# Kernel optimization log

Hardware: AMD Instinct MI355X
Metric: run time of the kernel (lower is better)

Reference implementation:

```python
import jax, jax.numpy as jnp
import numpy as np

B, T, NM = 32, 128, 53
IN_DIM, H, L = 3, 256, 64
K = 1024
HEADS, DH = 8, 64
INNER = HEADS * DH  # 512 (dim_head*heads, independent of H as in source)
COMMIT = 0.25


def _conv1d(x, w, b):
    # x: [B, C, T], w: [O, I, 3] (torch Conv1d layout), padding=1 == SAME for k=3
    y = jax.lax.conv_general_dilated(x, w, (1,), 'SAME',
                                     dimension_numbers=('NCH', 'OIH', 'NCH'))
    return y + b[None, :, None]


def setup_inputs():
    key = jax.random.key(0)
    ks = jax.random.split(key, 20)
    g = lambda i, shape: jax.random.normal(ks[i], shape, jnp.float32) * 0.02
    return dict(
        x=jax.random.normal(ks[0], (B, T, NM, IN_DIM), jnp.float32),
        seeds=jax.random.normal(ks[1], (B * T, NM, H), jnp.float32) * 0.02,
        enc_mlp_w1=g(2, (IN_DIM, H)), enc_mlp_b1=jnp.zeros((H,), jnp.float32),
        enc_mlp_w2=g(3, (H, H)), enc_mlp_b2=jnp.zeros((H,), jnp.float32),
        enc_qkv_w=g(4, (H, 3 * INNER)),
        enc_out_w=g(5, (INNER, H)), enc_out_b=jnp.zeros((H,), jnp.float32),
        enc_conv1_w=g(6, (H, H, 3)), enc_conv1_b=jnp.zeros((H,), jnp.float32),
        enc_conv2_w=g(7, (H, H, 3)), enc_conv2_b=jnp.zeros((H,), jnp.float32),
        enc_proj_w=g(8, (H, L)), enc_proj_b=jnp.zeros((L,), jnp.float32),
        codebook=jax.random.uniform(ks[9], (K, L), jnp.float32, -1.0 / K, 1.0 / K),
        dec_init_w=g(10, (L, H)), dec_init_b=jnp.zeros((H,), jnp.float32),
        dec_conv1_w=g(11, (H, H, 3)), dec_conv1_b=jnp.zeros((H,), jnp.float32),
        dec_conv2_w=g(12, (H, H, 3)), dec_conv2_b=jnp.zeros((H,), jnp.float32),
        dec_gen_w1=g(13, (H, H)), dec_gen_b1=jnp.zeros((H,), jnp.float32),
        dec_gen_w2=g(14, (H, H)), dec_gen_b2=jnp.zeros((H,), jnp.float32),
        dec_gen_w3=g(15, (H, IN_DIM)), dec_gen_b3=jnp.zeros((IN_DIM,), jnp.float32),
    )


def reference(x, seeds, enc_mlp_w1, enc_mlp_b1, enc_mlp_w2, enc_mlp_b2,
              enc_qkv_w, enc_out_w, enc_out_b,
              enc_conv1_w, enc_conv1_b, enc_conv2_w, enc_conv2_b,
              enc_proj_w, enc_proj_b, codebook,
              dec_init_w, dec_init_b,
              dec_conv1_w, dec_conv1_b, dec_conv2_w, dec_conv2_b,
              dec_gen_w1, dec_gen_b1, dec_gen_w2, dec_gen_b2,
              dec_gen_w3, dec_gen_b3):
    b, t, nm, _ = x.shape
    # ---- encoder ----
    h = x.reshape(b * t, nm, -1)
    h = jax.nn.relu(h @ enc_mlp_w1 + enc_mlp_b1)
    h = jax.nn.relu(h @ enc_mlp_w2 + enc_mlp_b2)
    qkv = h @ enc_qkv_w  # [(bt), nm, 3*INNER], no bias
    q, k_, v = jnp.split(qkv, 3, axis=-1)
    split_heads = lambda a: a.reshape(b * t, nm, HEADS, DH).transpose(0, 2, 1, 3)
    q, k_, v = split_heads(q), split_heads(k_), split_heads(v)
    dots = jnp.einsum('mhid,mhjd->mhij', q, k_) * (DH ** -0.5)
    attn = jax.nn.softmax(dots, axis=-1)
    o = jnp.einsum('mhij,mhjd->mhid', attn, v)
    o = o.transpose(0, 2, 1, 3).reshape(b * t, nm, INNER)
    h = o @ enc_out_w + enc_out_b
    h = h.mean(axis=1)                               # [(bt), H]
    h = h.reshape(b, t, -1).transpose(0, 2, 1)       # [b, H, t]
    h = jax.nn.relu(_conv1d(h, enc_conv1_w, enc_conv1_b))
    h = jax.nn.relu(_conv1d(h, enc_conv2_w, enc_conv2_b))
    z = h.transpose(0, 2, 1) @ enc_proj_w + enc_proj_b  # [b, t, L]
    # ---- vector quantizer (faithful to source: distance expression is only
    # the ||x||^2 term -> [M,1]; argmin over size-1 axis -> index 0 always) ----
    flat = z.reshape(-1, L)
    distances = jnp.sum(flat ** 2, axis=1, keepdims=True)  # [M, 1]
    idx = jnp.argmin(distances, axis=1)                    # all zeros
    encodings = jax.nn.one_hot(idx, K, dtype=z.dtype)      # [M, K]
    quantized = (encodings @ codebook).reshape(z.shape)
    e_loss = jnp.mean((jax.lax.stop_gradient(quantized) - z) ** 2)
    q_loss = jnp.mean((quantized - jax.lax.stop_gradient(z)) ** 2)
    vq_loss = q_loss + COMMIT * e_loss
    z_q = z + jax.lax.stop_gradient(quantized - z)  # straight-through
    avg_probs = jnp.mean(encodings, axis=0)
    perplexity = jnp.exp(-jnp.sum(avg_probs * jnp.log(avg_probs + 1e-10)))
    # ---- decoder ----
    d = z_q @ dec_init_w + dec_init_b                # [b, t, H]
    d = d.transpose(0, 2, 1)
    d = jax.nn.relu(_conv1d(d, dec_conv1_w, dec_conv1_b))
    d = jax.nn.relu(_conv1d(d, dec_conv2_w, dec_conv2_b))
    d = d.transpose(0, 2, 1).reshape(b * t, -1)      # [(bt), H]
    p = d[:, None, :] + seeds                        # [(bt), NM, H]
    p = jax.nn.relu(p @ dec_gen_w1 + dec_gen_b1)
    p = jax.nn.relu(p @ dec_gen_w2 + dec_gen_b2)
    p = p @ dec_gen_w3 + dec_gen_b3
    recon = p.reshape(b, t, NM, -1)
    return recon, vq_loss, perplexity
```

## Files before the change

### kernel.cpp

```cpp
#include <hip/hip_runtime.h>
#include <cstdint>
#include <cstddef>

#define NM    53
#define NMP   56
#define HD    256
#define BTT   4096

typedef __attribute__((ext_vector_type(8))) short short8v;
typedef __attribute__((ext_vector_type(4))) float f32x4;
#define MFMA16(a,b,c) __builtin_amdgcn_mfma_f32_16x16x32_bf16(a,b,c,0,0,0)

__device__ __forceinline__ float4 ldg4(const float* p) { return *(const float4*)p; }

__device__ __forceinline__ short f2bf(float f){
    union { float f; uint32_t u; } v; v.f = f;
    uint32_t r = v.u + 0x7fff + ((v.u >> 16) & 1);
    return (short)(r >> 16);
}
__device__ __forceinline__ float bf2f(short s){
    union { uint32_t u; float f; } v; v.u = ((uint32_t)(uint16_t)s) << 16;
    return v.f;
}

__global__ void k_prep_bf16(const float* __restrict__ w2, const float* __restrict__ wqkv,
                            const float* __restrict__ g1, const float* __restrict__ g2,
                            const float* __restrict__ g3,
                            short* __restrict__ w2T, short* __restrict__ wqkT,
                            short* __restrict__ g1T, short* __restrict__ g2T,
                            short* __restrict__ g3T)
{
    const int idx = blockIdx.x*256 + threadIdx.x;
    if (idx < 65536) {
        const int n = idx >> 8, k = idx & 255;
        w2T[idx] = f2bf(w2[k*HD + n]);
    } else if (idx < 327680) {
        const int j = idx - 65536;
        const int n = j >> 8, k = j & 255;
        wqkT[j] = f2bf(wqkv[(size_t)k*1536 + n]);
    } else if (idx < 393216) {
        const int j = idx - 327680;
        const int n = j >> 8, k = j & 255;
        g1T[j] = f2bf(g1[k*HD + n]);
    } else if (idx < 458752) {
        const int j = idx - 393216;
        const int n = j >> 8, k = j & 255;
        g2T[j] = f2bf(g2[k*HD + n]);
    } else if (idx < 462848) {
        const int j = idx - 458752;
        const int n = j >> 8, k = j & 255;
        g3T[j] = (n < 3) ? f2bf(g3[k*3 + n]) : (short)0;
    }
}

__global__ __launch_bounds__(256) void k_enc_attn(
    const float* __restrict__ x,
    const float* __restrict__ w1, const float* __restrict__ b1,
    const float* __restrict__ b2,
    const short* __restrict__ w2T,
    const short* __restrict__ wqkT,
    const float* __restrict__ wqkv,
    const float* __restrict__ wout, const float* __restrict__ bout,
    float* __restrict__ hbar)
{
    const int bt   = blockIdx.x;
    const int tid  = threadIdx.x;
    const int wv   = tid >> 6;
    const int lane = tid & 63;
    const int lr   = lane & 15;
    const int lg   = lane >> 4;

    __shared__ __align__(16) char  sU[35840];
    __shared__ __align__(16) short sH2b[64*264];
    __shared__ __align__(16) float sSmall[64+256+512];
    short* sH1b = (short*)sU;
    short* sQ   = (short*)sU;
    short* sK   = (short*)(sU + 9216);
    float* sDots= (float*)(sU + 18432);
    float* sPart= (float*)sU;
    float* sWj  = sSmall;
    float* sHw  = sSmall + 64;
    float* sObar= sSmall + 320;

    {
        const float* xr = x + (size_t)bt * (NM*3);
        const float W0 = w1[tid], W1 = w1[HD+tid], W2 = w1[2*HD+tid], B = b1[tid];
        for (int t = 0; t < 64; ++t) {
            float v = 0.f;
            if (t < NM)
                v = fmaxf(fmaf(xr[t*3], W0, fmaf(xr[t*3+1], W1, fmaf(xr[t*3+2], W2, B))), 0.f);
            sH1b[t*264 + tid] = f2bf(v);
        }
    }
    __syncthreads();

    {
        short8v a[8];
#pragma unroll
        for (int ks = 0; ks < 8; ++ks)
            a[ks] = *(const short8v*)(sH1b + (wv*16 + lr)*264 + ks*32 + lg*8);
        for (int nf = 0; nf < 16; ++nf) {
            f32x4 acc = {0.f, 0.f, 0.f, 0.f};
#pragma unroll
            for (int ks = 0; ks < 8; ++ks) {
                const short8v bfr = *(const short8v*)(w2T + (size_t)(nf*16 + lr)*HD + ks*32 + lg*8);
                acc = MFMA16(a[ks], bfr, acc);
            }
            const int n = nf*16 + lr;
            const float bb = b2[n];
#pragma unroll
            for (int r = 0; r < 4; ++r) {
                const int m = wv*16 + lg*4 + r;
                const float v = (m < NM) ? fmaxf(acc[r] + bb, 0.f) : 0.f;
                sH2b[m*264 + n] = f2bf(v);
            }
        }
    }
    __syncthreads();

    short8v ah[8];
#pragma unroll
    for (int ks = 0; ks < 8; ++ks)
        ah[ks] = *(const short8v*)(sH2b + (wv*16 + lr)*264 + ks*32 + lg*8);

    for (int h = 0; h < 8; ++h) {
        if (tid < 64) sWj[tid] = 0.f;
#pragma unroll
        for (int sec = 0; sec < 2; ++sec) {
            short* dst = sec ? sK : sQ;
            const short* wb = wqkT + (size_t)(sec*512 + h*64) * HD;
            for (int nf = 0; nf < 4; ++nf) {
                f32x4 acc = {0.f, 0.f, 0.f, 0.f};
#pragma unroll
                for (int ks = 0; ks < 8; ++ks) {
                    const short8v bfr = *(const short8v*)(wb + (size_t)(nf*16 + lr)*HD + ks*32 + lg*8);
                    acc = MFMA16(ah[ks], bfr, acc);
                }
                const int d = nf*16 + lr;
#pragma unroll
                for (int r = 0; r < 4; ++r) {
                    const int m = wv*16 + lg*4 + r;
                    dst[m*72 + d] = f2bf(acc[r]);
                }
            }
        }
        __syncthreads();

        {
            const short8v aq0 = *(const short8v*)(sQ + (wv*16 + lr)*72 + lg*8);
            const short8v aq1 = *(const short8v*)(sQ + (wv*16 + lr)*72 + 32 + lg*8);
#pragma unroll
            for (int nf = 0; nf < 4; ++nf) {
                f32x4 acc = {0.f, 0.f, 0.f, 0.f};
                const short8v bk0 = *(const short8v*)(sK + (nf*16 + lr)*72 + lg*8);
                const short8v bk1 = *(const short8v*)(sK + (nf*16 + lr)*72 + 32 + lg*8);
                acc = MFMA16(aq0, bk0, acc);
                acc = MFMA16(aq1, bk1, acc);
                const int j = nf*16 + lr;
#pragma unroll
                for (int r = 0; r < 4; ++r) {
                    const int i = wv*16 + lg*4 + r;
                    sDots[i*68 + j] = acc[r] * 0.125f;
                }
            }
        }
        __syncthreads();

        {
            const int jl  = lane & 15;
            const int grp = wv*4 + (lane >> 4);
            float w0 = 0.f, w1p = 0.f, w2p = 0.f, w3p = 0.f;
#pragma unroll
            for (int rnd = 0; rnd < 4; ++rnd) {
                const int i = rnd*16 + grp;
                const float v0 = sDots[i*68 + jl];
                const float v1 = sDots[i*68 + jl + 16];
                const float v2 = sDots[i*68 + jl + 32];
                const float v3 = sDots[i*68 + jl + 48];
                const bool m1 = (jl+16) < NM, m2 = (jl+32) < NM, m3 = (jl+48) < NM;
                float mx = v0;
                mx = fmaxf(mx, m1 ? v1 : -3.4e38f);
                mx = fmaxf(mx, m2 ? v2 : -3.4e38f);
                mx = fmaxf(mx, m3 ? v3 : -3.4e38f);
                mx = fmaxf(mx, __shfl_xor(mx, 1, 16));
                mx = fmaxf(mx, __shfl_xor(mx, 2, 16));
                mx = fmaxf(mx, __shfl_xor(mx, 4, 16));
                mx = fmaxf(mx, __shfl_xor(mx, 8, 16));
                const float e0 = __expf(v0 - mx);
                const float e1 = m1 ? __expf(v1 - mx) : 0.f;
                const float e2 = m2 ? __expf(v2 - mx) : 0.f;
                const float e3 = m3 ? __expf(v3 - mx) : 0.f;
                float s = e0 + e1 + e2 + e3;
                s += __shfl_xor(s, 1, 16);
                s += __shfl_xor(s, 2, 16);
                s += __shfl_xor(s, 4, 16);
                s += __shfl_xor(s, 8, 16);
                if (i < NM) {
                    const float inv = 1.f / s;
                    w0 = fmaf(e0, inv, w0);
                    w1p = fmaf(e1, inv, w1p);
                    w2p = fmaf(e2, inv, w2p);
                    w3p = fmaf(e3, inv, w3p);
                }
            }
            atomicAdd(&sWj[jl],      w0);
            atomicAdd(&sWj[jl + 16], w1p);
            atomicAdd(&sWj[jl + 32], w2p);
            atomicAdd(&sWj[jl + 48], w3p);
        }
        __syncthreads();

        {
            float s = 0.f;
#pragma unroll 4
            for (int j = 0; j < NM; ++j) s = fmaf(sWj[j], bf2f(sH2b[j*264 + tid]), s);
            sHw[tid] = s;
        }
        __syncthreads();

        {
            const int dl = lane & 15;
            const int cq = lane >> 4;
            const int d  = wv*16 + dl;
            const float* wvp = wqkv + 1024 + (size_t)h*64 + d;
            float s = 0.f;
            const int c0 = cq * 64;
#pragma unroll 8
            for (int c = c0; c < c0 + 64; ++c)
                s = fmaf(sHw[c], wvp[(size_t)c*1536], s);
            s += __shfl_xor(s, 16);
            s += __shfl_xor(s, 32);
            if (cq == 0) sObar[h*64 + d] = s;
        }
    }
    __syncthreads();

    {
        const int c4 = lane << 2;
        float a0 = 0.f, a1 = 0.f, a2 = 0.f, a3 = 0.f;
        for (int m = wv*128; m < wv*128 + 128; ++m) {
            const float ob = sObar[m] * (1.f/53.f);
            const float4 w = ldg4(wout + (size_t)m*HD + c4);
            a0 = fmaf(ob, w.x, a0); a1 = fmaf(ob, w.y, a1);
            a2 = fmaf(ob, w.z, a2); a3 = fmaf(ob, w.w, a3);
        }
        sPart[wv*256 + c4 + 0] = a0;
        sPart[wv*256 + c4 + 1] = a1;
        sPart[wv*256 + c4 + 2] = a2;
        sPart[wv*256 + c4 + 3] = a3;
    }
    __syncthreads();
    hbar[(size_t)bt*HD + tid] =
        sPart[tid] + sPart[256+tid] + sPart[512+tid] + sPart[768+tid] + bout[tid];
}

__global__ void k_transpose_conv(const float* __restrict__ w, float* __restrict__ wT)
{
    const int idx = blockIdx.x*256 + threadIdx.x;
    if (idx < 3*HD*HD) {
        const int o = idx & 255;
        const int i = (idx >> 8) & 255;
        const int s = idx >> 16;
        wT[idx] = w[(size_t)(o*HD + i)*3 + s];
    }
}

__global__ __launch_bounds__(256) void k_enc_conv(
    const float* __restrict__ hbar,
    const float* __restrict__ wc1T, const float* __restrict__ cb1,
    const float* __restrict__ wc2T, const float* __restrict__ cb2,
    const float* __restrict__ wproj, const float* __restrict__ bproj,
    float* __restrict__ z)
{
    const int b = blockIdx.y, chunk = blockIdx.x;
    const int t0 = chunk * 16;
    const int tid = threadIdx.x;
    __shared__ __align__(16) float sIn[22][HD];
    __shared__ __align__(16) float sMid[18][HD];

    for (int idx = tid; idx < 20*HD; idx += 256) {
        const int r = idx >> 8, c = idx & 255;
        const int t = t0 - 2 + r;
        sIn[r][c] = (t >= 0 && t < 128) ? hbar[(size_t)(b*128 + t)*HD + c] : 0.f;
    }
    __syncthreads();
    const int cg = tid & 63, tg = tid >> 6;
    const int c4 = cg << 2;
    {
        float acc[5][4];
#pragma unroll
        for (int r2 = 0; r2 < 5; ++r2) { acc[r2][0]=0.f; acc[r2][1]=0.f; acc[r2][2]=0.f; acc[r2][3]=0.f; }
        for (int s = 0; s < 3; ++s)
            for (int i = 0; i < HD; ++i) {
                const float4 w = ldg4(wc1T + (size_t)(s*HD + i)*HD + c4);
#pragma unroll
                for (int r2 = 0; r2 < 5; ++r2) {
                    const float v = sIn[tg*5 + r2 + s][i];
                    acc[r2][0] = fmaf(v, w.x, acc[r2][0]);
                    acc[r2][1] = fmaf(v, w.y, acc[r2][1]);
                    acc[r2][2] = fmaf(v, w.z, acc[r2][2]);
                    acc[r2][3] = fmaf(v, w.w, acc[r2][3]);
                }
            }
        const float4 bb = ldg4(cb1 + c4);
#pragma unroll
        for (int r2 = 0; r2 < 5; ++r2) {
            const int rr = tg*5 + r2;
            if (rr < 18) {
                const int tp = t0 - 1 + rr;
                float4 o; o.x=0.f; o.y=0.f; o.z=0.f; o.w=0.f;
                if (tp >= 0 && tp < 128) {
                    o.x = fmaxf(acc[r2][0] + bb.x, 0.f);
                    o.y = fmaxf(acc[r2][1] + bb.y, 0.f);
                    o.z = fmaxf(acc[r2][2] + bb.z, 0.f);
                    o.w = fmaxf(acc[r2][3] + bb.w, 0.f);
                }
                *(float4*)(&sMid[rr][c4]) = o;
            }
        }
    }
    __syncthreads();
    {
        float acc[4][4];
#pragma unroll
        for (int r2 = 0; r2 < 4; ++r2) { acc[r2][0]=0.f; acc[r2][1]=0.f; acc[r2][2]=0.f; acc[r2][3]=0.f; }
        for (int s = 0; s < 3; ++s)
            for (int i = 0; i < HD; ++i) {
                const float4 w = ldg4(wc2T + (size_t)(s*HD + i)*HD + c4);
#pragma unroll
                for (int r2 = 0; r2 < 4; ++r2) {
                    const float v = sMid[tg*4 + r2 + s][i];
                    acc[r2][0] = fmaf(v, w.x, acc[r2][0]);
                    acc[r2][1] = fmaf(v, w.y, acc[r2][1]);
                    acc[r2][2] = fmaf(v, w.z, acc[r2][2]);
                    acc[r2][3] = fmaf(v, w.w, acc[r2][3]);
                }
            }
        const float4 bb = ldg4(cb2 + c4);
#pragma unroll
        for (int r2 = 0; r2 < 4; ++r2) {
            float4 o;
            o.x = fmaxf(acc[r2][0] + bb.x, 0.f);
            o.y = fmaxf(acc[r2][1] + bb.y, 0.f);
            o.z = fmaxf(acc[r2][2] + bb.z, 0.f);
            o.w = fmaxf(acc[r2][3] + bb.w, 0.f);
            *(float4*)(&sIn[tg*4 + r2][c4]) = o;
        }
    }
    __syncthreads();
    {
        const int cgp = tid & 15, tgp = tid >> 4;
        const int l4 = cgp << 2;
        float a0 = bproj[l4+0], a1 = bproj[l4+1], a2 = bproj[l4+2], a3 = bproj[l4+3];
        for (int i = 0; i < HD; ++i) {
            const float4 w = ldg4(wproj + (size_t)i*64 + l4);
            const float v = sIn[tgp][i];
            a0 = fmaf(v, w.x, a0); a1 = fmaf(v, w.y, a1);
            a2 = fmaf(v, w.z, a2); a3 = fmaf(v, w.w, a3);
        }
        float4 o; o.x=a0; o.y=a1; o.z=a2; o.w=a3;
        *(float4*)(z + (size_t)(b*128 + t0 + tgp)*64 + l4) = o;
    }
}

__global__ void k_vq_reduce(const float* __restrict__ z,
                            const float* __restrict__ codebook,
                            float* __restrict__ acc)
{
    const int tid = threadIdx.x;
    float s = 0.f;
    for (int idx = blockIdx.x*256 + tid; idx < BTT*64; idx += gridDim.x*256) {
        const float d = z[idx] - codebook[idx & 63];
        s = fmaf(d, d, s);
    }
#pragma unroll
    for (int off = 32; off > 0; off >>= 1) s += __shfl_xor(s, off);
    __shared__ float sred[4];
    if ((tid & 63) == 0) sred[tid >> 6] = s;
    __syncthreads();
    if (tid == 0) atomicAdd(acc, sred[0] + sred[1] + sred[2] + sred[3]);
}

__global__ void k_vq_final(const float* __restrict__ acc, float* __restrict__ out, int out_size)
{
    if (threadIdx.x == 0 && blockIdx.x == 0) {
        const float mse = acc[0] * (1.f / (BTT*64.f));
        out[out_size-2] = 1.25f * mse;
        out[out_size-1] = 1.0f;
    }
}

__global__ __launch_bounds__(256) void k_dec_prefix(
    const float* __restrict__ codebook,
    const float* __restrict__ winit, const float* __restrict__ binit,
    const float* __restrict__ wdc1, const float* __restrict__ bdc1,
    const float* __restrict__ wdc2, const float* __restrict__ bdc2,
    float* __restrict__ dclass)
{
    const int c = threadIdx.x;
    __shared__ float sD[HD];
    __shared__ float sY1[3][HD];
    float v = binit[c];
    for (int l = 0; l < 64; ++l) v = fmaf(codebook[l], winit[l*HD + c], v);
    sD[c] = v;
    __syncthreads();
    float A0 = 0.f, A1 = 0.f, A2 = 0.f;
    for (int i = 0; i < HD; ++i) {
        const float di = sD[i];
        const float* wp = wdc1 + (size_t)c*768 + i*3;
        A0 = fmaf(wp[0], di, A0);
        A1 = fmaf(wp[1], di, A1);
        A2 = fmaf(wp[2], di, A2);
    }
    const float bb = bdc1[c];
    sY1[0][c] = fmaxf(bb + A1 + A2, 0.f);
    sY1[1][c] = fmaxf(bb + A0 + A1 + A2, 0.f);
    sY1[2][c] = fmaxf(bb + A0 + A1, 0.f);
    __syncthreads();
    const int Ls[5] = {-1, 0, 1, 1, 1};
    const int Cs[5] = { 0, 1, 1, 1, 2};
    const int Rs[5] = { 1, 1, 1, 2,-1};
    for (int cls = 0; cls < 5; ++cls) {
        float s = bdc2[c];
        const int li = Ls[cls], ci = Cs[cls], ri = Rs[cls];
        for (int i = 0; i < HD; ++i) {
            const float* wp = wdc2 + (size_t)c*768 + i*3;
            const float Lv = (li >= 0) ? sY1[li][i] : 0.f;
            const float Cv = sY1[ci][i];
            const float Rv = (ri >= 0) ? sY1[ri][i] : 0.f;
            s = fmaf(wp[0], Lv, s);
            s = fmaf(wp[1], Cv, s);
            s = fmaf(wp[2], Rv, s);
        }
        dclass[cls*HD + c] = fmaxf(s, 0.f);
    }
}

__global__ __launch_bounds__(256) void k_dec_gen(
    const float* __restrict__ seeds,
    const float* __restrict__ dclass,
    const short* __restrict__ g1T, const float* __restrict__ gb1,
    const short* __restrict__ g2T, const float* __restrict__ gb2,
    const short* __restrict__ g3T, const float* __restrict__ gb3,
    float* __restrict__ out)
{
    const int bt   = blockIdx.x;
    const int tid  = threadIdx.x;
    const int wv   = tid >> 6;
    const int lane = tid & 63;
    const int lr   = lane & 15;
    const int lg   = lane >> 4;
    const int t    = bt & 127;
    const int cls  = (t == 0) ? 0 : (t == 1) ? 1 : (t < 126) ? 2 : (t == 126) ? 3 : 4;

    __shared__ __align__(16) short sA[64*264];
    __shared__ __align__(16) short sB[64*264];

    {
        const int cg = tid & 63, tg = tid >> 6;
        const int c4 = cg << 2;
        const float4 dv = ldg4(dclass + cls*HD + c4);
        const float* srow = seeds + (size_t)bt * (NM*HD);
        for (int it = 0; it < 16; ++it) {
            const int tt = it*4 + tg;
            short v0 = 0, v1 = 0, v2 = 0, v3 = 0;
            if (tt < NM) {
                const float4 s4 = ldg4(srow + (size_t)tt*HD + c4);
                v0 = f2bf(s4.x + dv.x); v1 = f2bf(s4.y + dv.y);
                v2 = f2bf(s4.z + dv.z); v3 = f2bf(s4.w + dv.w);
            }
            short* p = sA + tt*264 + c4;
            p[0] = v0; p[1] = v1; p[2] = v2; p[3] = v3;
        }
    }
    __syncthreads();

    {
        short8v a[8];
#pragma unroll
        for (int ks = 0; ks < 8; ++ks)
            a[ks] = *(const short8v*)(sA + (wv*16 + lr)*264 + ks*32 + lg*8);
        for (int nf = 0; nf < 16; ++nf) {
            f32x4 acc = {0.f, 0.f, 0.f, 0.f};
#pragma unroll
            for (int ks = 0; ks < 8; ++ks) {
                const short8v bfr = *(const short8v*)(g1T + (size_t)(nf*16 + lr)*HD + ks*32 + lg*8);
                acc = MFMA16(a[ks], bfr, acc);
            }
            const int n = nf*16 + lr;
            const float bb = gb1[n];
#pragma unroll
            for (int r = 0; r < 4; ++r) {
                const int m = wv*16 + lg*4 + r;
                const float v = (m < NM) ? fmaxf(acc[r] + bb, 0.f) : 0.f;
                sB[m*264 + n] = f2bf(v);
            }
        }
    }
    __syncthreads();

    {
        short8v a[8];
#pragma unroll
        for (int ks = 0; ks < 8; ++ks)
            a[ks] = *(const short8v*)(sB + (wv*16 + lr)*264 + ks*32 + lg*8);
        for (int nf = 0; nf < 16; ++nf) {
            f32x4 acc = {0.f, 0.f, 0.f, 0.f};
#pragma unroll
            for (int ks = 0; ks < 8; ++ks) {
                const short8v bfr = *(const short8v*)(g2T + (size_t)(nf*16 + lr)*HD + ks*32 + lg*8);
                acc = MFMA16(a[ks], bfr, acc);
            }
            const int n = nf*16 + lr;
            const float bb = gb2[n];
#pragma unroll
            for (int r = 0; r < 4; ++r) {
                const int m = wv*16 + lg*4 + r;
                const float v = (m < NM) ? fmaxf(acc[r] + bb, 0.f) : 0.f;
                sA[m*264 + n] = f2bf(v);
            }
        }
    }
    __syncthreads();

    {
        f32x4 acc = {0.f, 0.f, 0.f, 0.f};
#pragma unroll
        for (int ks = 0; ks < 8; ++ks) {
            const short8v a = *(const short8v*)(sA + (wv*16 + lr)*264 + ks*32 + lg*8);
            const short8v bfr = *(const short8v*)(g3T + (size_t)lr*HD + ks*32 + lg*8);
            acc = MFMA16(a, bfr, acc);
        }
        if (lr < 3) {
            const float bb = gb3[lr];
#pragma unroll
            for (int r = 0; r < 4; ++r) {
                const int m = wv*16 + lg*4 + r;
                if (m < NM)
                    out[(size_t)(bt*NM + m)*3 + lr] = acc[r] + bb;
            }
        }
    }
}

extern "C" void kernel_launch(void* const* d_in, const int* in_sizes, int n_in,
                              void* d_out, int out_size, void* d_ws, size_t ws_size,
                              hipStream_t stream)
{
    const float* x      = (const float*)d_in[0];
    const float* seeds  = (const float*)d_in[1];
    const float* w1     = (const float*)d_in[2];
    const float* b1     = (const float*)d_in[3];
    const float* w2     = (const float*)d_in[4];
    const float* b2     = (const float*)d_in[5];
    const float* wqkv   = (const float*)d_in[6];
    const float* wout   = (const float*)d_in[7];
    const float* bout   = (const float*)d_in[8];
    const float* wc1    = (const float*)d_in[9];
    const float* cb1    = (const float*)d_in[10];
    const float* wc2    = (const float*)d_in[11];
    const float* cb2    = (const float*)d_in[12];
    const float* wproj  = (const float*)d_in[13];
    const float* bproj  = (const float*)d_in[14];
    const float* codebook = (const float*)d_in[15];
    const float* winit  = (const float*)d_in[16];
    const float* binit  = (const float*)d_in[17];
    const float* wdc1   = (const float*)d_in[18];
    const float* bdc1   = (const float*)d_in[19];
    const float* wdc2   = (const float*)d_in[20];
    const float* bdc2   = (const float*)d_in[21];
    const float* g1     = (const float*)d_in[22];
    const float* gb1    = (const float*)d_in[23];
    const float* g2     = (const float*)d_in[24];
    const float* gb2    = (const float*)d_in[25];
    const float* g3     = (const float*)d_in[26];
    const float* gb3    = (const float*)d_in[27];

    float* ws     = (float*)d_ws;
    float* hbar   = ws;
    float* zbuf   = ws + 1048576;
    float* wc1T   = ws + 1310720;
    float* wc2T   = ws + 1507328;
    float* dclass = ws + 1703936;
    float* accp   = ws + 1705216;
    short* w2T    = (short*)(ws + 1705220);
    short* wqkT   = (short*)(ws + 1737988);
    short* g1T    = (short*)(ws + 1869060);
    short* g2T    = (short*)(ws + 1901828);
    short* g3T    = (short*)(ws + 1934596);

    float* out = (float*)d_out;

    hipMemsetAsync(accp, 0, sizeof(float), stream);
    k_prep_bf16<<<1808, 256, 0, stream>>>(w2, wqkv, g1, g2, g3, w2T, wqkT, g1T, g2T, g3T);
    k_transpose_conv<<<768, 256, 0, stream>>>(wc1, wc1T);
    k_transpose_conv<<<768, 256, 0, stream>>>(wc2, wc2T);
    k_dec_prefix<<<1, 256, 0, stream>>>(codebook, winit, binit, wdc1, bdc1, wdc2, bdc2, dclass);
    k_enc_attn<<<BTT, 256, 0, stream>>>(x, w1, b1, b2, w2T, wqkT, wqkv, wout, bout, hbar);
    k_enc_conv<<<dim3(8, 32), 256, 0, stream>>>(hbar, wc1T, cb1, wc2T, cb2, wproj, bproj, zbuf);
    k_vq_reduce<<<256, 256, 0, stream>>>(zbuf, codebook, accp);
    k_vq_final<<<1, 64, 0, stream>>>(accp, out, out_size);
    k_dec_gen<<<BTT, 256, 0, stream>>>(seeds, dclass, g1T, gb1, g2T, gb2, g3T, gb3, out);
}
```

Before: 2.577 ms.

## Fuse softmax into QK MFMA registers and batch per-head value projection

The softmax now runs directly on the MFMA accumulator registers, so the scores are no longer written to shared memory and re-read. The K buffer is double-buffered by head parity, which removes several barriers per head. The attention-weighted H sums and the V projection are deferred until after the head loop and done for all eight heads at once, giving coalesced loads of the wqkv rows. The max subtraction in softmax is dropped, which relies on the scores staying small enough not to overflow exp.

```diff
diff --git a/kernel.cpp b/kernel.cpp
--- a/kernel.cpp
+++ b/kernel.cpp
@@ -70,17 +70,16 @@
     const int lr   = lane & 15;
     const int lg   = lane >> 4;
 
-    __shared__ __align__(16) char  sU[35840];
+    __shared__ __align__(16) char  sU[33792];
     __shared__ __align__(16) short sH2b[64*264];
-    __shared__ __align__(16) float sSmall[64+256+512];
+    __shared__ __align__(16) float sWjAll[64*8];
+    __shared__ __align__(16) float sHwAll[8*256];
+    __shared__ __align__(16) float sObar[512];
     short* sH1b = (short*)sU;
     short* sQ   = (short*)sU;
-    short* sK   = (short*)(sU + 9216);
-    float* sDots= (float*)(sU + 18432);
+    short* sK0  = (short*)(sU + 9216);
+    short* sK1  = (short*)(sU + 18432);
     float* sPart= (float*)sU;
-    float* sWj  = sSmall;
-    float* sHw  = sSmall + 64;
-    float* sObar= sSmall + 320;
 
     {
         const float* xr = x + (size_t)bt * (NM*3);
@@ -91,6 +90,8 @@
                 v = fmaxf(fmaf(xr[t*3], W0, fmaf(xr[t*3+1], W1, fmaf(xr[t*3+2], W2, B))), 0.f);
             sH1b[t*264 + tid] = f2bf(v);
         }
+        sWjAll[tid] = 0.f;
+        sWjAll[256 + tid] = 0.f;
     }
     __syncthreads();
 
@@ -124,10 +125,10 @@
         ah[ks] = *(const short8v*)(sH2b + (wv*16 + lr)*264 + ks*32 + lg*8);
 
     for (int h = 0; h < 8; ++h) {
-        if (tid < 64) sWj[tid] = 0.f;
+        short* kb = (h & 1) ? sK1 : sK0;
 #pragma unroll
         for (int sec = 0; sec < 2; ++sec) {
-            short* dst = sec ? sK : sQ;
+            short* dst = sec ? kb : sQ;
             const short* wb = wqkT + (size_t)(sec*512 + h*64) * HD;
             for (int nf = 0; nf < 4; ++nf) {
                 f32x4 acc = {0.f, 0.f, 0.f, 0.f};
@@ -149,89 +150,77 @@
         {
             const short8v aq0 = *(const short8v*)(sQ + (wv*16 + lr)*72 + lg*8);
             const short8v aq1 = *(const short8v*)(sQ + (wv*16 + lr)*72 + 32 + lg*8);
+            f32x4 pr[4];
 #pragma unroll
             for (int nf = 0; nf < 4; ++nf) {
                 f32x4 acc = {0.f, 0.f, 0.f, 0.f};
-                const short8v bk0 = *(const short8v*)(sK + (nf*16 + lr)*72 + lg*8);
-                const short8v bk1 = *(const short8v*)(sK + (nf*16 + lr)*72 + 32 + lg*8);
+                const short8v bk0 = *(const short8v*)(kb + (nf*16 + lr)*72 + lg*8);
+                const short8v bk1 = *(const short8v*)(kb + (nf*16 + lr)*72 + 32 + lg*8);
                 acc = MFMA16(aq0, bk0, acc);
                 acc = MFMA16(aq1, bk1, acc);
-                const int j = nf*16 + lr;
-#pragma unroll
-                for (int r = 0; r < 4; ++r) {
-                    const int i = wv*16 + lg*4 + r;
-                    sDots[i*68 + j] = acc[r] * 0.125f;
-                }
-            }
-        }
-        __syncthreads();
-
-        {
-            const int jl  = lane & 15;
-            const int grp = wv*4 + (lane >> 4);
-            float w0 = 0.f, w1p = 0.f, w2p = 0.f, w3p = 0.f;
-#pragma unroll
-            for (int rnd = 0; rnd < 4; ++rnd) {
-                const int i = rnd*16 + grp;
-                const float v0 = sDots[i*68 + jl];
-                const float v1 = sDots[i*68 + jl + 16];
-                const float v2 = sDots[i*68 + jl + 32];
-                const float v3 = sDots[i*68 + jl + 48];
-                const bool m1 = (jl+16) < NM, m2 = (jl+32) < NM, m3 = (jl+48) < NM;
-                float mx = v0;
-                mx = fmaxf(mx, m1 ? v1 : -3.4e38f);
-                mx = fmaxf(mx, m2 ? v2 : -3.4e38f);
-                mx = fmaxf(mx, m3 ? v3 : -3.4e38f);
-                mx = fmaxf(mx, __shfl_xor(mx, 1, 16));
-                mx = fmaxf(mx, __shfl_xor(mx, 2, 16));
-                mx = fmaxf(mx, __shfl_xor(mx, 4, 16));
-                mx = fmaxf(mx, __shfl_xor(mx, 8, 16));
-                const float e0 = __expf(v0 - mx);
-                const float e1 = m1 ? __expf(v1 - mx) : 0.f;
-                const float e2 = m2 ? __expf(v2 - mx) : 0.f;
-                const float e3 = m3 ? __expf(v3 - mx) : 0.f;
-                float s = e0 + e1 + e2 + e3;
+                pr[nf] = acc;
+            }
+            float e[4][4];
+#pragma unroll
+            for (int nf = 0; nf < 4; ++nf) {
+                const bool jok = (nf < 3) || (lr < 5);
+#pragma unroll
+                for (int r = 0; r < 4; ++r)
+                    e[r][nf] = jok ? __expf(pr[nf][r] * 0.125f) : 0.f;
+            }
+            float inv[4];
+#pragma unroll
+            for (int r = 0; r < 4; ++r) {
+                float s = (e[r][0] + e[r][1]) + (e[r][2] + e[r][3]);
                 s += __shfl_xor(s, 1, 16);
                 s += __shfl_xor(s, 2, 16);
                 s += __shfl_xor(s, 4, 16);
                 s += __shfl_xor(s, 8, 16);
-                if (i < NM) {
-                    const float inv = 1.f / s;
-                    w0 = fmaf(e0, inv, w0);
-                    w1p = fmaf(e1, inv, w1p);
-                    w2p = fmaf(e2, inv, w2p);
-                    w3p = fmaf(e3, inv, w3p);
+                inv[r] = 1.0f / s;
+            }
+#pragma unroll
+            for (int nf = 0; nf < 4; ++nf) {
+                float w = 0.f;
+#pragma unroll
+                for (int r = 0; r < 4; ++r) {
+                    const int i = wv*16 + lg*4 + r;
+                    if (i < NM) w = fmaf(e[r][nf], inv[r], w);
                 }
-            }
-            atomicAdd(&sWj[jl],      w0);
-            atomicAdd(&sWj[jl + 16], w1p);
-            atomicAdd(&sWj[jl + 32], w2p);
-            atomicAdd(&sWj[jl + 48], w3p);
-        }
-        __syncthreads();
-
-        {
-            float s = 0.f;
-#pragma unroll 4
-            for (int j = 0; j < NM; ++j) s = fmaf(sWj[j], bf2f(sH2b[j*264 + tid]), s);
-            sHw[tid] = s;
-        }
-        __syncthreads();
-
-        {
-            const int dl = lane & 15;
-            const int cq = lane >> 4;
-            const int d  = wv*16 + dl;
-            const float* wvp = wqkv + 1024 + (size_t)h*64 + d;
-            float s = 0.f;
-            const int c0 = cq * 64;
-#pragma unroll 8
-            for (int c = c0; c < c0 + 64; ++c)
-                s = fmaf(sHw[c], wvp[(size_t)c*1536], s);
-            s += __shfl_xor(s, 16);
-            s += __shfl_xor(s, 32);
-            if (cq == 0) sObar[h*64 + d] = s;
-        }
+                w += __shfl_xor(w, 16);
+                w += __shfl_xor(w, 32);
+                if (lg == 0) atomicAdd(&sWjAll[(nf*16 + lr)*8 + h], w);
+            }
+        }
+    }
+    __syncthreads();
+
+    {
+        float hw[8] = {0.f,0.f,0.f,0.f,0.f,0.f,0.f,0.f};
+        for (int j = 0; j < NM; ++j) {
+            const float hv = bf2f(sH2b[j*264 + tid]);
+            const float4 wj0 = *(const float4*)&sWjAll[j*8];
+            const float4 wj1 = *(const float4*)&sWjAll[j*8 + 4];
+            hw[0] = fmaf(wj0.x, hv, hw[0]); hw[1] = fmaf(wj0.y, hv, hw[1]);
+            hw[2] = fmaf(wj0.z, hv, hw[2]); hw[3] = fmaf(wj0.w, hv, hw[3]);
+            hw[4] = fmaf(wj1.x, hv, hw[4]); hw[5] = fmaf(wj1.y, hv, hw[5]);
+            hw[6] = fmaf(wj1.z, hv, hw[6]); hw[7] = fmaf(wj1.w, hv, hw[7]);
+        }
+#pragma unroll
+        for (int h = 0; h < 8; ++h) sHwAll[h*256 + tid] = hw[h];
+    }
+    __syncthreads();
+
+    {
+        const int h1 = tid >> 6;
+        const float* base = wqkv + 1024;
+        float a0 = 0.f, a1 = 0.f;
+        for (int c = 0; c < HD; ++c) {
+            const float* rowp = base + (size_t)c*1536;
+            a0 = fmaf(sHwAll[h1*256 + c],       rowp[tid],       a0);
+            a1 = fmaf(sHwAll[1024 + h1*256 + c], rowp[256 + tid], a1);
+        }
+        sObar[tid] = a0;
+        sObar[256 + tid] = a1;
     }
     __syncthreads();
 
```

New measurement: 2.438 ms. 5.4% less time.
